# Kernel tuning notes

Measured on AMD Instinct MI355X. Metric: run time of the kernel, lower is better.

The kernel has to match this reference:

```python
import jax, jax.numpy as jnp
import numpy as np

H = 16  # n_heads


def setup_inputs() -> dict:
    key = jax.random.key(0)
    ks = jax.random.split(key, 12)
    B, S, D = 16, 512, 1024
    inp = {
        "query": jax.random.normal(ks[0], (B, S, D), jnp.float32),
        "key": jax.random.normal(ks[1], (B, S, D), jnp.float32),
        "value": jax.random.normal(ks[2], (B, S, D), jnp.float32),
        "mask": jnp.ones((B, S), dtype=bool),
        "adj": jax.random.uniform(ks[3], (B, S, S), jnp.float32),
        # nn.Linear weights are [out, in]; y = x @ W.T + b
        "Wq": jax.random.normal(ks[4], (D, D), jnp.float32) / np.sqrt(D),
        "bq": jnp.zeros((D,), jnp.float32),
        "Wk": jax.random.normal(ks[5], (D, D), jnp.float32) / np.sqrt(D),
        "bk": jnp.zeros((D,), jnp.float32),
        "Wv": jax.random.normal(ks[6], (D, D), jnp.float32) / np.sqrt(D),
        "bv": jnp.zeros((D,), jnp.float32),
        "Wo": jax.random.normal(ks[7], (D, D), jnp.float32) / np.sqrt(D),
        "bo": jnp.zeros((D,), jnp.float32),
        "beta": jnp.array([0.5], jnp.float32),  # learned residual scale (init 0 in torch)
    }
    return inp


def reference(query, key, value, mask, adj, Wq, bq, Wk, bk, Wv, bv, Wo, bo, beta):
    B, S, D = query.shape
    h = H
    dk = D // h
    N = S * dk  # channel-attention "sequence" length

    def proj(x, W, b):
        # [B,S,D] -> [B,h,S,dk]
        return (x @ W.T + b).reshape(B, S, h, dk).transpose(0, 2, 1, 3)

    Q = proj(query, Wq, bq)
    K = proj(key, Wk, bk)
    V = proj(value, Wv, bv)

    # Flatten each head: [B, h, S*dk]; torch's q,k,v are the [B,N,h] transposes.
    Qf = Q.reshape(B, h, N)
    Kf = K.reshape(B, h, N)
    Vf = V.reshape(B, h, N)

    # channel attention: scores = q^T k / sqrt(h) -> [B,h,h]
    scores = jnp.einsum("bin,bjn->bij", Qf, Kf) / jnp.sqrt(jnp.asarray(h, Qf.dtype))
    attn = jax.nn.softmax(scores, axis=-1)  # dropout is identity at eval

    # x2 = attn @ v^T -> [B,h,N] -> view [B,h,S,dk]
    x2 = jnp.einsum("bij,bjn->bin", attn, Vf).reshape(B, h, S, dk)

    x = V + beta * x2                      # scaled residual on value
    x = x.transpose(0, 2, 1, 3).reshape(B, S, D)
    out = x @ Wo.T + bo
    return out, attn
```

## Files before the change

### kernel.cpp

```cpp
#include <hip/hip_runtime.h>
#include <cstdint>
#include <cstddef>


#define DIM 1024

typedef _Float16 f16_t;
typedef _Float16 f16x4_t __attribute__((ext_vector_type(4)));
typedef _Float16 f16x8_t __attribute__((ext_vector_type(8)));
typedef float    f32x4_t __attribute__((ext_vector_type(4)));

__device__ __forceinline__ void async_ld16(const void* g, void* l) {
    __builtin_amdgcn_global_load_lds((const __attribute__((address_space(1))) void*)g,
                                     (__attribute__((address_space(3))) void*)l,
                                     16, 0, 0);
}

__global__ __launch_bounds__(256) void pack_kernel(
    const float* __restrict__ q, const float* __restrict__ k, const float* __restrict__ v,
    const float* __restrict__ Wq, const float* __restrict__ Wk,
    const float* __restrict__ Wv, const float* __restrict__ Wo,
    f16_t* __restrict__ Aq, f16_t* __restrict__ Ak, f16_t* __restrict__ Av,
    f16_t* __restrict__ Bq, f16_t* __restrict__ Bk,
    f16_t* __restrict__ Bv, f16_t* __restrict__ Bo,
    float* __restrict__ scores)
{
    const int u = blockIdx.x * 256 + threadIdx.x;
    if (u >= 7340032) {
        scores[u - 7340032] = 0.f;
        return;
    }
    const float* src; f16_t* dst; int i;
    if (u < 2097152)      { src = q;  dst = Aq; i = u; }
    else if (u < 4194304) { src = k;  dst = Ak; i = u - 2097152; }
    else if (u < 6291456) { src = v;  dst = Av; i = u - 4194304; }
    else if (u < 6553600) { src = Wq; dst = Bq; i = u - 6291456; }
    else if (u < 6815744) { src = Wk; dst = Bk; i = u - 6553600; }
    else if (u < 7077888) { src = Wv; dst = Bv; i = u - 6815744; }
    else                  { src = Wo; dst = Bo; i = u - 7077888; }
    float4 s = ((const float4*)src)[i];
    f16x4_t h;
    h[0] = (f16_t)s.x; h[1] = (f16_t)s.y; h[2] = (f16_t)s.z; h[3] = (f16_t)s.w;
    ((f16x4_t*)dst)[i] = h;
}

__device__ __forceinline__ void gemm_body(
    const f16_t* __restrict__ A, const f16_t* __restrict__ B,
    const float* __restrict__ bias, float* __restrict__ C, f16_t* __restrict__ C16,
    f16_t* As, f16_t* Bs, int tileM, int tileN)
{
    const int tid  = threadIdx.x;
    const int lane = tid & 63;
    const int w    = tid >> 6;
    const int wm = (w & 1) << 6;
    const int wn = (w >> 1) << 6;

    f32x4_t acc[4][4];
#pragma unroll
    for (int i = 0; i < 4; ++i)
#pragma unroll
        for (int j = 0; j < 4; ++j)
            acc[i][j] = (f32x4_t){0.f, 0.f, 0.f, 0.f};

    const int srow = lane >> 3;
    const int scol = ((lane & 7) ^ (lane >> 3)) << 3;
    const int arow = lane & 15;
    const int sx   = lane & 7;
    const int kqu  = lane >> 4;

    for (int kt = 0; kt < 16; ++kt) {
        const int k0 = kt << 6;
#pragma unroll
        for (int t = 0; t < 4; ++t) {
            const int row = (w << 5) + (t << 3);
            async_ld16(A + (size_t)(tileM + row + srow) * DIM + k0 + scol,
                       (void*)(As + row * 64));
            async_ld16(B + (size_t)(tileN + row + srow) * DIM + k0 + scol,
                       (void*)(Bs + row * 64));
        }
        __syncthreads();
#pragma unroll
        for (int kk = 0; kk < 2; ++kk) {
            const int cu = ((kk << 2) + kqu) ^ sx;
            f16x8_t af[4], bfv[4];
#pragma unroll
            for (int mt = 0; mt < 4; ++mt)
                af[mt] = *(const f16x8_t*)(As + (wm + (mt << 4) + arow) * 64 + (cu << 3));
#pragma unroll
            for (int nt = 0; nt < 4; ++nt)
                bfv[nt] = *(const f16x8_t*)(Bs + (wn + (nt << 4) + arow) * 64 + (cu << 3));
#pragma unroll
            for (int mt = 0; mt < 4; ++mt)
#pragma unroll
                for (int nt = 0; nt < 4; ++nt)
                    acc[mt][nt] = __builtin_amdgcn_mfma_f32_16x16x32_f16(
                        af[mt], bfv[nt], acc[mt][nt], 0, 0, 0);
        }
        __syncthreads();
    }

    const int rq = (lane >> 4) << 2;
    if (C16) {
#pragma unroll
        for (int nt = 0; nt < 4; ++nt) {
            const int col = tileN + wn + (nt << 4) + arow;
            const float bv = bias[col];
#pragma unroll
            for (int mt = 0; mt < 4; ++mt) {
                const int row = tileM + wm + (mt << 4) + rq;
#pragma unroll
                for (int r = 0; r < 4; ++r)
                    C16[(size_t)(row + r) * DIM + col] = (f16_t)(acc[mt][nt][r] + bv);
            }
        }
    } else {
#pragma unroll
        for (int nt = 0; nt < 4; ++nt) {
            const int col = tileN + wn + (nt << 4) + arow;
            const float bv = bias[col];
#pragma unroll
            for (int mt = 0; mt < 4; ++mt) {
                const int row = tileM + wm + (mt << 4) + rq;
#pragma unroll
                for (int r = 0; r < 4; ++r)
                    C[(size_t)(row + r) * DIM + col] = acc[mt][nt][r] + bv;
            }
        }
    }
}

struct Gemm3Args {
    const f16_t* A[3];
    const f16_t* B[3];
    const float* bias[3];
    float*       C[3];
    f16_t*       C16[3];
};

__global__ __launch_bounds__(256) void gemm3(Gemm3Args args)
{
    __shared__ __align__(16) f16_t As[128 * 64];
    __shared__ __align__(16) f16_t Bs[128 * 64];
    const int z = blockIdx.z;
    gemm_body(args.A[z], args.B[z], args.bias[z], args.C[z], args.C16[z],
              As, Bs, blockIdx.x * 128, blockIdx.y * 128);
}

__global__ __launch_bounds__(256) void gemm_f16(
    const f16_t* __restrict__ A, const f16_t* __restrict__ B,
    const float* __restrict__ bias, float* __restrict__ C)
{
    __shared__ __align__(16) f16_t As[128 * 64];
    __shared__ __align__(16) f16_t Bs[128 * 64];
    gemm_body(A, B, bias, C, nullptr, As, Bs, blockIdx.x * 128, blockIdx.y * 128);
}

__global__ __launch_bounds__(256) void scores_kernel(
    const f16_t* __restrict__ Pq16, const f16_t* __restrict__ Pk16,
    float* __restrict__ scores)
{
    __shared__ float red[4][256];
    const int b = blockIdx.x;
    const int lane = threadIdx.x & 63;
    const int w = threadIdx.x >> 6;
    const int m  = lane & 15;
    const int q8 = (lane >> 4) << 3;

    f32x4_t acc = (f32x4_t){0.f, 0.f, 0.f, 0.f};
    const int s0 = blockIdx.y * 16 + w * 4;
#pragma unroll
    for (int ss = 0; ss < 4; ++ss) {
        const size_t rb = (size_t)(b * 512 + s0 + ss) * DIM;
        const f16_t* qrow = Pq16 + rb;
        const f16_t* krow = Pk16 + rb;
#pragma unroll
        for (int c0 = 0; c0 < 64; c0 += 32) {
            f16x8_t af = *(const f16x8_t*)(qrow + m * 64 + c0 + q8);
            f16x8_t bf = *(const f16x8_t*)(krow + m * 64 + c0 + q8);
            acc = __builtin_amdgcn_mfma_f32_16x16x32_f16(af, bf, acc, 0, 0, 0);
        }
    }
    const int rq = (lane >> 4) << 2;
#pragma unroll
    for (int r = 0; r < 4; ++r)
        red[w][(rq + r) * 16 + m] = acc[r];
    __syncthreads();
    const int t = threadIdx.x;
    const float sum = red[0][t] + red[1][t] + red[2][t] + red[3][t];
    atomicAdd(&scores[b * 256 + t], sum);
}

__global__ __launch_bounds__(256) void softmax_kernel(
    const float* __restrict__ scores, const float* __restrict__ beta_p,
    float* __restrict__ attn_out, float* __restrict__ Mm)
{
    const int t = threadIdx.x;
    const int i = t & 15;
    const float beta = beta_p[0];
    float s[16];
    float mx = -1e30f;
#pragma unroll
    for (int j = 0; j < 16; ++j) {
        s[j] = scores[t * 16 + j] * 0.25f;
        mx = fmaxf(mx, s[j]);
    }
    float sum = 0.f;
#pragma unroll
    for (int j = 0; j < 16; ++j) { s[j] = expf(s[j] - mx); sum += s[j]; }
    const float inv = 1.f / sum;
#pragma unroll
    for (int j = 0; j < 16; ++j) {
        float a = s[j] * inv;
        attn_out[t * 16 + j] = a;
        Mm[t * 16 + j] = beta * a + ((j == i) ? 1.f : 0.f);
    }
}

__global__ __launch_bounds__(256) void mix_kernel(
    const float* __restrict__ Pv, const float* __restrict__ Mm,
    f16_t* __restrict__ xmix)
{
    __shared__ float Msh[256];
    const int rbase = blockIdx.x * 8;
    const int b = rbase >> 9;
    Msh[threadIdx.x] = Mm[b * 256 + threadIdx.x];
    __syncthreads();
    const int w = threadIdx.x >> 6;
    const int lane = threadIdx.x & 63;
#pragma unroll
    for (int rr = 0; rr < 2; ++rr) {
        const int r = rbase + w * 2 + rr;
        const float* vrow = Pv + (size_t)r * DIM;
        float v[16];
#pragma unroll
        for (int j = 0; j < 16; ++j) v[j] = vrow[j * 64 + lane];
#pragma unroll
        for (int i = 0; i < 16; ++i) {
            float x = 0.f;
#pragma unroll
            for (int j = 0; j < 16; ++j) x += Msh[i * 16 + j] * v[j];
            xmix[(size_t)r * DIM + i * 64 + lane] = (f16_t)x;
        }
    }
}

extern "C" void kernel_launch(void* const* d_in, const int* in_sizes, int n_in,
                              void* d_out, int out_size, void* d_ws, size_t ws_size,
                              hipStream_t stream)
{
    (void)in_sizes; (void)n_in; (void)out_size; (void)ws_size;
    const float* q    = (const float*)d_in[0];
    const float* k    = (const float*)d_in[1];
    const float* v    = (const float*)d_in[2];
    const float* Wq   = (const float*)d_in[5];
    const float* bq   = (const float*)d_in[6];
    const float* Wk   = (const float*)d_in[7];
    const float* bk   = (const float*)d_in[8];
    const float* Wv   = (const float*)d_in[9];
    const float* bv   = (const float*)d_in[10];
    const float* Wo   = (const float*)d_in[11];
    const float* bo   = (const float*)d_in[12];
    const float* beta = (const float*)d_in[13];

    float* out  = (float*)d_out;
    float* attn = (float*)d_out + 8388608;

    char* p = (char*)d_ws;
    auto take = [&](size_t n) -> char* {
        char* cur = p; p += (n + 255) & ~(size_t)255; return cur;
    };
    f16_t* Aq = (f16_t*)take(16777216);
    f16_t* Ak = (f16_t*)take(16777216);
    f16_t* Av = (f16_t*)take(16777216);
    f16_t* Bq = (f16_t*)take(2097152);
    f16_t* Bk = (f16_t*)take(2097152);
    f16_t* Bv = (f16_t*)take(2097152);
    f16_t* Bo = (f16_t*)take(2097152);
    f16_t* Pq16 = (f16_t*)take(16777216);
    f16_t* Pk16 = (f16_t*)take(16777216);
    float* Pv = (float*)take(33554432);
    float* scores = (float*)take(16384);
    float* Mm     = (float*)take(16384);
    f16_t* xmix = Aq;

    pack_kernel<<<28688, 256, 0, stream>>>(q, k, v, Wq, Wk, Wv, Wo,
                                           Aq, Ak, Av, Bq, Bk, Bv, Bo, scores);

    Gemm3Args ga;
    ga.A[0] = Aq; ga.A[1] = Ak; ga.A[2] = Av;
    ga.B[0] = Bq; ga.B[1] = Bk; ga.B[2] = Bv;
    ga.bias[0] = bq; ga.bias[1] = bk; ga.bias[2] = bv;
    ga.C[0] = nullptr; ga.C[1] = nullptr; ga.C[2] = Pv;
    ga.C16[0] = Pq16; ga.C16[1] = Pk16; ga.C16[2] = nullptr;
    gemm3<<<dim3(64, 8, 3), 256, 0, stream>>>(ga);

    scores_kernel<<<dim3(16, 32), 256, 0, stream>>>(Pq16, Pk16, scores);
    softmax_kernel<<<1, 256, 0, stream>>>(scores, beta, attn, Mm);
    mix_kernel<<<1024, 256, 0, stream>>>(Pv, Mm, xmix);
    gemm_f16<<<dim3(64, 8), 256, 0, stream>>>(xmix, Bo, bo, out);
}
```

Before: 293.2 us.

## Replace QKV projection GEMM with 256x256 double-buffered phased pipeline

The fused Q/K/V projection GEMM moves from 128x128 tiles with 256 threads and a single LDS buffer to 256x256 tiles with 512 threads. It double-buffers the k-slices in 128 KB of LDS and splits each k-step into four load/MFMA phases. Async global-to-LDS loads for the next tile are interleaved with MFMA work under barriers and priority hints, with explicit vmcnt waits. The aim is to hide memory latency and raise data reuse per tile, at the cost of heavier register use, larger LDS footprint, lower occupancy and fewer blocks (384) to fill the CUs.

```diff
diff --git a/kernel.cpp b/kernel.cpp
--- a/kernel.cpp
+++ b/kernel.cpp
@@ -44,69 +44,136 @@
     ((f16x4_t*)dst)[i] = h;
 }
 
-__device__ __forceinline__ void gemm_body(
-    const f16_t* __restrict__ A, const f16_t* __restrict__ B,
+__device__ __forceinline__ void gemm256_body(
+    const f16_t* __restrict__ A, const f16_t* __restrict__ Bm,
     const float* __restrict__ bias, float* __restrict__ C, f16_t* __restrict__ C16,
-    f16_t* As, f16_t* Bs, int tileM, int tileN)
+    f16_t* lds, int tileM, int tileN)
 {
     const int tid  = threadIdx.x;
     const int lane = tid & 63;
     const int w    = tid >> 6;
-    const int wm = (w & 1) << 6;
-    const int wn = (w >> 1) << 6;
-
-    f32x4_t acc[4][4];
-#pragma unroll
-    for (int i = 0; i < 4; ++i)
+    const int wm   = (w & 1) << 7;
+    const int wn   = (w >> 1) << 6;
+    const int lr   = lane & 15;
+    const int cu   = lane >> 4;
+    const int up   = (((lr & 1) << 2) | cu) ^ (lr >> 1);
+    const int abase = ((w & 1) << 12) + ((lr >> 1) << 6) + (up << 3);
+    const int bbase = ((w >> 1) << 11) + ((lr >> 1) << 6) + (up << 3);
+
+    const int su   = (tid & 7) ^ ((tid >> 3) & 7);
+    const int srow = ((tid >> 3) << 1) | (su >> 2);
+    const int sk   = (su & 3) << 3;
+    const f16_t* srcA = A  + (size_t)(tileM + srow) * DIM + sk;
+    const f16_t* srcB = Bm + (size_t)(tileN + srow) * DIM + sk;
+    f16_t* dstW = lds + (w << 9);
+
+#define STG(mat, kk, c, kt, b)  async_ld16( \
+        ((mat) ? srcB : srcA) + (size_t)(c) * 128 * DIM + (kt) * 64 + (kk) * 32, \
+        dstW + (b) * 32768 + (mat) * 16384 + (kk) * 8192 + (c) * 4096)
+
+    f32x4_t acc[8][4];
+#pragma unroll
+    for (int i = 0; i < 8; ++i)
 #pragma unroll
         for (int j = 0; j < 4; ++j)
             acc[i][j] = (f32x4_t){0.f, 0.f, 0.f, 0.f};
 
-    const int srow = lane >> 3;
-    const int scol = ((lane & 7) ^ (lane >> 3)) << 3;
-    const int arow = lane & 15;
-    const int sx   = lane & 7;
-    const int kqu  = lane >> 4;
-
+    STG(0,0,0, 0,0); STG(0,0,1, 0,0);
+    STG(1,0,0, 0,0); STG(1,0,1, 0,0);
+    STG(0,1,0, 0,0); STG(0,1,1, 0,0);
+    STG(1,1,0, 0,0); STG(1,1,1, 0,0);
+    asm volatile("s_waitcnt vmcnt(4)" ::: "memory");
+    __builtin_amdgcn_s_barrier();
+    __builtin_amdgcn_sched_barrier(0);
+
+#pragma unroll 2
     for (int kt = 0; kt < 16; ++kt) {
-        const int k0 = kt << 6;
-#pragma unroll
-        for (int t = 0; t < 4; ++t) {
-            const int row = (w << 5) + (t << 3);
-            async_ld16(A + (size_t)(tileM + row + srow) * DIM + k0 + scol,
-                       (void*)(As + row * 64));
-            async_ld16(B + (size_t)(tileN + row + srow) * DIM + k0 + scol,
-                       (void*)(Bs + row * 64));
-        }
-        __syncthreads();
-#pragma unroll
-        for (int kk = 0; kk < 2; ++kk) {
-            const int cu = ((kk << 2) + kqu) ^ sx;
-            f16x8_t af[4], bfv[4];
-#pragma unroll
-            for (int mt = 0; mt < 4; ++mt)
-                af[mt] = *(const f16x8_t*)(As + (wm + (mt << 4) + arow) * 64 + (cu << 3));
+        const int b  = kt & 1;
+        const int nb = b ^ 1;
+        const f16_t* Lb = lds + b * 32768;
+        f16x8_t af[4], bf[4];
+
+#pragma unroll
+        for (int nt = 0; nt < 4; ++nt)
+            bf[nt] = *(const f16x8_t*)(Lb + 16384 + bbase + (nt << 9));
+#pragma unroll
+        for (int mt = 0; mt < 4; ++mt)
+            af[mt] = *(const f16x8_t*)(Lb + abase + (mt << 9));
+        if (kt < 15) { STG(0,0,0, kt+1, nb); STG(0,0,1, kt+1, nb); }
+        __builtin_amdgcn_s_barrier();
+        __builtin_amdgcn_s_setprio(1);
+#pragma unroll
+        for (int mt = 0; mt < 4; ++mt)
 #pragma unroll
             for (int nt = 0; nt < 4; ++nt)
-                bfv[nt] = *(const f16x8_t*)(Bs + (wn + (nt << 4) + arow) * 64 + (cu << 3));
-#pragma unroll
-            for (int mt = 0; mt < 4; ++mt)
-#pragma unroll
-                for (int nt = 0; nt < 4; ++nt)
-                    acc[mt][nt] = __builtin_amdgcn_mfma_f32_16x16x32_f16(
-                        af[mt], bfv[nt], acc[mt][nt], 0, 0, 0);
-        }
-        __syncthreads();
-    }
+                acc[mt][nt] = __builtin_amdgcn_mfma_f32_16x16x32_f16(
+                    af[mt], bf[nt], acc[mt][nt], 0, 0, 0);
+        __builtin_amdgcn_s_setprio(0);
+        __builtin_amdgcn_s_barrier();
+
+#pragma unroll
+        for (int mt = 0; mt < 4; ++mt)
+            af[mt] = *(const f16x8_t*)(Lb + abase + ((mt + 4) << 9));
+        if (kt < 15) { STG(1,0,0, kt+1, nb); STG(1,0,1, kt+1, nb); }
+        __builtin_amdgcn_s_barrier();
+        __builtin_amdgcn_s_setprio(1);
+#pragma unroll
+        for (int mt = 0; mt < 4; ++mt)
+#pragma unroll
+            for (int nt = 0; nt < 4; ++nt)
+                acc[mt + 4][nt] = __builtin_amdgcn_mfma_f32_16x16x32_f16(
+                    af[mt], bf[nt], acc[mt + 4][nt], 0, 0, 0);
+        __builtin_amdgcn_s_setprio(0);
+        if (kt < 15) asm volatile("s_waitcnt vmcnt(4)" ::: "memory");
+        else         asm volatile("s_waitcnt vmcnt(0)" ::: "memory");
+        __builtin_amdgcn_s_barrier();
+        __builtin_amdgcn_sched_barrier(0);
+
+#pragma unroll
+        for (int nt = 0; nt < 4; ++nt)
+            bf[nt] = *(const f16x8_t*)(Lb + 24576 + bbase + (nt << 9));
+#pragma unroll
+        for (int mt = 0; mt < 4; ++mt)
+            af[mt] = *(const f16x8_t*)(Lb + 8192 + abase + (mt << 9));
+        if (kt < 15) { STG(0,1,0, kt+1, nb); STG(0,1,1, kt+1, nb); }
+        __builtin_amdgcn_s_barrier();
+        __builtin_amdgcn_s_setprio(1);
+#pragma unroll
+        for (int mt = 0; mt < 4; ++mt)
+#pragma unroll
+            for (int nt = 0; nt < 4; ++nt)
+                acc[mt][nt] = __builtin_amdgcn_mfma_f32_16x16x32_f16(
+                    af[mt], bf[nt], acc[mt][nt], 0, 0, 0);
+        __builtin_amdgcn_s_setprio(0);
+        __builtin_amdgcn_s_barrier();
+
+#pragma unroll
+        for (int mt = 0; mt < 4; ++mt)
+            af[mt] = *(const f16x8_t*)(Lb + 8192 + abase + ((mt + 4) << 9));
+        if (kt < 15) { STG(1,1,0, kt+1, nb); STG(1,1,1, kt+1, nb); }
+        __builtin_amdgcn_s_barrier();
+        __builtin_amdgcn_s_setprio(1);
+#pragma unroll
+        for (int mt = 0; mt < 4; ++mt)
+#pragma unroll
+            for (int nt = 0; nt < 4; ++nt)
+                acc[mt + 4][nt] = __builtin_amdgcn_mfma_f32_16x16x32_f16(
+                    af[mt], bf[nt], acc[mt + 4][nt], 0, 0, 0);
+        __builtin_amdgcn_s_setprio(0);
+        if (kt < 15) asm volatile("s_waitcnt vmcnt(4)" ::: "memory");
+        __builtin_amdgcn_s_barrier();
+        __builtin_amdgcn_sched_barrier(0);
+    }
+#undef STG
 
     const int rq = (lane >> 4) << 2;
     if (C16) {
 #pragma unroll
         for (int nt = 0; nt < 4; ++nt) {
-            const int col = tileN + wn + (nt << 4) + arow;
+            const int col = tileN + wn + (nt << 4) + lr;
             const float bv = bias[col];
 #pragma unroll
-            for (int mt = 0; mt < 4; ++mt) {
+            for (int mt = 0; mt < 8; ++mt) {
                 const int row = tileM + wm + (mt << 4) + rq;
 #pragma unroll
                 for (int r = 0; r < 4; ++r)
@@ -116,10 +183,10 @@
     } else {
 #pragma unroll
         for (int nt = 0; nt < 4; ++nt) {
-            const int col = tileN + wn + (nt << 4) + arow;
+            const int col = tileN + wn + (nt << 4) + lr;
             const float bv = bias[col];
 #pragma unroll
-            for (int mt = 0; mt < 4; ++mt) {
+            for (int mt = 0; mt < 8; ++mt) {
                 const int row = tileM + wm + (mt << 4) + rq;
 #pragma unroll
                 for (int r = 0; r < 4; ++r)
@@ -137,13 +204,82 @@
     f16_t*       C16[3];
 };
 
-__global__ __launch_bounds__(256) void gemm3(Gemm3Args args)
-{
-    __shared__ __align__(16) f16_t As[128 * 64];
-    __shared__ __align__(16) f16_t Bs[128 * 64];
+__global__ __launch_bounds__(512, 2) void gemm3_8ph(Gemm3Args args)
+{
+    __shared__ __align__(16) f16_t lds[65536];
     const int z = blockIdx.z;
-    gemm_body(args.A[z], args.B[z], args.bias[z], args.C[z], args.C16[z],
-              As, Bs, blockIdx.x * 128, blockIdx.y * 128);
+    gemm256_body(args.A[z], args.B[z], args.bias[z], args.C[z], args.C16[z],
+                 lds, blockIdx.x * 256, blockIdx.y * 256);
+}
+
+__device__ __forceinline__ void gemm_body(
+    const f16_t* __restrict__ A, const f16_t* __restrict__ B,
+    const float* __restrict__ bias, float* __restrict__ C, f16_t* __restrict__ C16,
+    f16_t* As, f16_t* Bs, int tileM, int tileN)
+{
+    const int tid  = threadIdx.x;
+    const int lane = tid & 63;
+    const int w    = tid >> 6;
+    const int wm = (w & 1) << 6;
+    const int wn = (w >> 1) << 6;
+
+    f32x4_t acc[4][4];
+#pragma unroll
+    for (int i = 0; i < 4; ++i)
+#pragma unroll
+        for (int j = 0; j < 4; ++j)
+            acc[i][j] = (f32x4_t){0.f, 0.f, 0.f, 0.f};
+
+    const int srow = lane >> 3;
+    const int scol = ((lane & 7) ^ (lane >> 3)) << 3;
+    const int arow = lane & 15;
+    const int sx   = lane & 7;
+    const int kqu  = lane >> 4;
+
+    for (int kt = 0; kt < 16; ++kt) {
+        const int k0 = kt << 6;
+#pragma unroll
+        for (int t = 0; t < 4; ++t) {
+            const int row = (w << 5) + (t << 3);
+            async_ld16(A + (size_t)(tileM + row + srow) * DIM + k0 + scol,
+                       (void*)(As + row * 64));
+            async_ld16(B + (size_t)(tileN + row + srow) * DIM + k0 + scol,
+                       (void*)(Bs + row * 64));
+        }
+        __syncthreads();
+#pragma unroll
+        for (int kk = 0; kk < 2; ++kk) {
+            const int cuv = ((kk << 2) + kqu) ^ sx;
+            f16x8_t af[4], bfv[4];
+#pragma unroll
+            for (int mt = 0; mt < 4; ++mt)
+                af[mt] = *(const f16x8_t*)(As + (wm + (mt << 4) + arow) * 64 + (cuv << 3));
+#pragma unroll
+            for (int nt = 0; nt < 4; ++nt)
+                bfv[nt] = *(const f16x8_t*)(Bs + (wn + (nt << 4) + arow) * 64 + (cuv << 3));
+#pragma unroll
+            for (int mt = 0; mt < 4; ++mt)
+#pragma unroll
+                for (int nt = 0; nt < 4; ++nt)
+                    acc[mt][nt] = __builtin_amdgcn_mfma_f32_16x16x32_f16(
+                        af[mt], bfv[nt], acc[mt][nt], 0, 0, 0);
+        }
+        __syncthreads();
+    }
+
+    const int rq = (lane >> 4) << 2;
+#pragma unroll
+    for (int nt = 0; nt < 4; ++nt) {
+        const int col = tileN + wn + (nt << 4) + arow;
+        const float bv = bias[col];
+#pragma unroll
+        for (int mt = 0; mt < 4; ++mt) {
+            const int row = tileM + wm + (mt << 4) + rq;
+#pragma unroll
+            for (int r = 0; r < 4; ++r)
+                C[(size_t)(row + r) * DIM + col] = acc[mt][nt][r] + bv;
+        }
+    }
 }
 
 __global__ __launch_bounds__(256) void gemm_f16(
@@ -292,7 +428,7 @@
     ga.bias[0] = bq; ga.bias[1] = bk; ga.bias[2] = bv;
     ga.C[0] = nullptr; ga.C[1] = nullptr; ga.C[2] = Pv;
     ga.C16[0] = Pq16; ga.C16[1] = Pk16; ga.C16[2] = nullptr;
-    gemm3<<<dim3(64, 8, 3), 256, 0, stream>>>(ga);
+    gemm3_8ph<<<dim3(32, 4, 3), 512, 0, stream>>>(ga);
 
     scores_kernel<<<dim3(16, 32), 256, 0, stream>>>(Pq16, Pk16, scores);
     softmax_kernel<<<1, 256, 0, stream>>>(scores, beta, attn, Mm);
```

New measurement: 295.5 us. Within noise of the previous version (+0.8%).

## Replace GEMM with 256x128 tile, 4-stage async LDS pipeline and 512 threads

Applied to the files above, without the earlier changes.

Rewrites the shared GEMM body to use 256x128 block tiles with 8 waves, a K-step of 32 and a four-buffer ring of async global-to-LDS loads issued three stages ahead. Explicit vmcnt waits replace the double __syncthreads per iteration, leaving a single barrier per step, and s_setprio raises wave priority around the MFMA block. The intent is to overlap global memory latency with MFMA work and raise arithmetic intensity per block. In exchange it uses more LDS per block, hand-coded waitcnt logic that depends on exact load counts, and half as many blocks per grid.

```diff
diff --git a/kernel.cpp b/kernel.cpp
--- a/kernel.cpp
+++ b/kernel.cpp
@@ -44,16 +44,30 @@
     ((f16x4_t*)dst)[i] = h;
 }
 
-__device__ __forceinline__ void gemm_body(
-    const f16_t* __restrict__ A, const f16_t* __restrict__ B,
+__device__ __forceinline__ void gemm256x128_body(
+    const f16_t* __restrict__ A, const f16_t* __restrict__ Bm,
     const float* __restrict__ bias, float* __restrict__ C, f16_t* __restrict__ C16,
-    f16_t* As, f16_t* Bs, int tileM, int tileN)
-{
-    const int tid  = threadIdx.x;
-    const int lane = tid & 63;
-    const int w    = tid >> 6;
-    const int wm = (w & 1) << 6;
-    const int wn = (w >> 1) << 6;
+    int tileM, int tileN)
+{
+    __shared__ __align__(16) f16_t As0[8192], As1[8192], As2[8192], As3[8192];
+    __shared__ __align__(16) f16_t Bs0[4096], Bs1[4096], Bs2[4096], Bs3[4096];
+
+    const int t    = threadIdx.x;
+    const int lane = t & 63;
+    const int w    = t >> 6;
+
+    const int srow = t >> 2;
+    const int su   = (t & 3) ^ (((t >> 2) ^ (t >> 4)) & 3);
+    const f16_t* srcA = A  + (size_t)(tileM + srow) * DIM + su * 8;
+    const f16_t* srcB = Bm + (size_t)(tileN + srow) * DIM + su * 8;
+
+    const int lr = lane & 15;
+    const int ku = lane >> 4;
+    const int uA = ku ^ ((lr ^ (lr >> 2)) & 3);
+    const int mr = w >> 1;
+    const int nr = w & 1;
+    const int aOff = mr * 2048 + lr * 32 + uA * 8;
+    const int bOff = nr * 2048 + lr * 32 + uA * 8;
 
     f32x4_t acc[4][4];
 #pragma unroll
@@ -62,52 +76,67 @@
         for (int j = 0; j < 4; ++j)
             acc[i][j] = (f32x4_t){0.f, 0.f, 0.f, 0.f};
 
-    const int srow = lane >> 3;
-    const int scol = ((lane & 7) ^ (lane >> 3)) << 3;
-    const int arow = lane & 15;
-    const int sx   = lane & 7;
-    const int kqu  = lane >> 4;
-
-    for (int kt = 0; kt < 16; ++kt) {
-        const int k0 = kt << 6;
-#pragma unroll
-        for (int t = 0; t < 4; ++t) {
-            const int row = (w << 5) + (t << 3);
-            async_ld16(A + (size_t)(tileM + row + srow) * DIM + k0 + scol,
-                       (void*)(As + row * 64));
-            async_ld16(B + (size_t)(tileN + row + srow) * DIM + k0 + scol,
-                       (void*)(Bs + row * 64));
-        }
-        __syncthreads();
-#pragma unroll
-        for (int kk = 0; kk < 2; ++kk) {
-            const int cu = ((kk << 2) + kqu) ^ sx;
-            f16x8_t af[4], bfv[4];
-#pragma unroll
-            for (int mt = 0; mt < 4; ++mt)
-                af[mt] = *(const f16x8_t*)(As + (wm + (mt << 4) + arow) * 64 + (cu << 3));
-#pragma unroll
-            for (int nt = 0; nt < 4; ++nt)
-                bfv[nt] = *(const f16x8_t*)(Bs + (wn + (nt << 4) + arow) * 64 + (cu << 3));
-#pragma unroll
-            for (int mt = 0; mt < 4; ++mt)
-#pragma unroll
-                for (int nt = 0; nt < 4; ++nt)
-                    acc[mt][nt] = __builtin_amdgcn_mfma_f32_16x16x32_f16(
-                        af[mt], bfv[nt], acc[mt][nt], 0, 0, 0);
-        }
-        __syncthreads();
-    }
-
-    const int rq = (lane >> 4) << 2;
+#define STAGE(KT, AP, BP) do {                                              \
+        const f16_t* ga_ = srcA + (KT) * 32;                                \
+        async_ld16(ga_,             (void*)((AP) + (w << 9)));              \
+        async_ld16(ga_ + 128 * DIM, (void*)((AP) + (w << 9) + 4096));       \
+        async_ld16(srcB + (KT) * 32,(void*)((BP) + (w << 9)));              \
+    } while (0)
+
+#define ITER(KT, AP, BP, PAP, PBP) do {                                     \
+        f16x8_t af_[4], bf_[4];                                             \
+        _Pragma("unroll")                                                   \
+        for (int mt = 0; mt < 4; ++mt)                                      \
+            af_[mt] = *(const f16x8_t*)((AP) + aOff + (mt << 9));           \
+        _Pragma("unroll")                                                   \
+        for (int nt = 0; nt < 4; ++nt)                                      \
+            bf_[nt] = *(const f16x8_t*)((BP) + bOff + (nt << 9));           \
+        if ((KT) < 29) STAGE((KT) + 3, PAP, PBP);                           \
+        __builtin_amdgcn_s_setprio(1);                                      \
+        _Pragma("unroll")                                                   \
+        for (int mt = 0; mt < 4; ++mt)                                      \
+        _Pragma("unroll")                                                   \
+        for (int nt = 0; nt < 4; ++nt)                                      \
+            acc[mt][nt] = __builtin_amdgcn_mfma_f32_16x16x32_f16(           \
+                af_[mt], bf_[nt], acc[mt][nt], 0, 0, 0);                    \
+        __builtin_amdgcn_s_setprio(0);                                      \
+        if ((KT) <= 28)      asm volatile("s_waitcnt vmcnt(6)" ::: "memory"); \
+        else if ((KT) == 29) asm volatile("s_waitcnt vmcnt(3)" ::: "memory"); \
+        else if ((KT) == 30) asm volatile("s_waitcnt vmcnt(0)" ::: "memory"); \
+        if ((KT) < 31) {                                                    \
+            __builtin_amdgcn_s_barrier();                                   \
+            __builtin_amdgcn_sched_barrier(0);                              \
+        }                                                                   \
+    } while (0)
+
+    STAGE(0, As0, Bs0);
+    STAGE(1, As1, Bs1);
+    STAGE(2, As2, Bs2);
+    asm volatile("s_waitcnt vmcnt(6)" ::: "memory");
+    __builtin_amdgcn_s_barrier();
+    __builtin_amdgcn_sched_barrier(0);
+
+#define QUAD(K0)                                   \
+    ITER((K0) + 0, As0, Bs0, As3, Bs3);            \
+    ITER((K0) + 1, As1, Bs1, As0, Bs0);            \
+    ITER((K0) + 2, As2, Bs2, As1, Bs1);            \
+    ITER((K0) + 3, As3, Bs3, As2, Bs2);
+
+    QUAD(0) QUAD(4) QUAD(8) QUAD(12) QUAD(16) QUAD(20) QUAD(24) QUAD(28)
+
+#undef QUAD
+#undef ITER
+#undef STAGE
+
+    const int rq = ku << 2;
     if (C16) {
 #pragma unroll
         for (int nt = 0; nt < 4; ++nt) {
-            const int col = tileN + wn + (nt << 4) + arow;
+            const int col = tileN + nr * 64 + (nt << 4) + lr;
             const float bv = bias[col];
 #pragma unroll
             for (int mt = 0; mt < 4; ++mt) {
-                const int row = tileM + wm + (mt << 4) + rq;
+                const int row = tileM + mr * 64 + (mt << 4) + rq;
 #pragma unroll
                 for (int r = 0; r < 4; ++r)
                     C16[(size_t)(row + r) * DIM + col] = (f16_t)(acc[mt][nt][r] + bv);
@@ -116,11 +145,11 @@
     } else {
 #pragma unroll
         for (int nt = 0; nt < 4; ++nt) {
-            const int col = tileN + wn + (nt << 4) + arow;
+            const int col = tileN + nr * 64 + (nt << 4) + lr;
             const float bv = bias[col];
 #pragma unroll
             for (int mt = 0; mt < 4; ++mt) {
-                const int row = tileM + wm + (mt << 4) + rq;
+                const int row = tileM + mr * 64 + (mt << 4) + rq;
 #pragma unroll
                 for (int r = 0; r < 4; ++r)
                     C[(size_t)(row + r) * DIM + col] = acc[mt][nt][r] + bv;
@@ -137,22 +166,18 @@
     f16_t*       C16[3];
 };
 
-__global__ __launch_bounds__(256) void gemm3(Gemm3Args args)
-{
-    __shared__ __align__(16) f16_t As[128 * 64];
-    __shared__ __align__(16) f16_t Bs[128 * 64];
+__global__ __launch_bounds__(512, 2) void gemm3(Gemm3Args args)
+{
     const int z = blockIdx.z;
-    gemm_body(args.A[z], args.B[z], args.bias[z], args.C[z], args.C16[z],
-              As, Bs, blockIdx.x * 128, blockIdx.y * 128);
-}
-
-__global__ __launch_bounds__(256) void gemm_f16(
+    gemm256x128_body(args.A[z], args.B[z], args.bias[z], args.C[z], args.C16[z],
+                     blockIdx.x * 256, blockIdx.y * 128);
+}
+
+__global__ __launch_bounds__(512, 2) void gemm_o(
     const f16_t* __restrict__ A, const f16_t* __restrict__ B,
     const float* __restrict__ bias, float* __restrict__ C)
 {
-    __shared__ __align__(16) f16_t As[128 * 64];
-    __shared__ __align__(16) f16_t Bs[128 * 64];
-    gemm_body(A, B, bias, C, nullptr, As, Bs, blockIdx.x * 128, blockIdx.y * 128);
+    gemm256x128_body(A, B, bias, C, nullptr, blockIdx.x * 256, blockIdx.y * 128);
 }
 
 __global__ __launch_bounds__(256) void scores_kernel(
@@ -185,9 +210,9 @@
     for (int r = 0; r < 4; ++r)
         red[w][(rq + r) * 16 + m] = acc[r];
     __syncthreads();
-    const int t = threadIdx.x;
-    const float sum = red[0][t] + red[1][t] + red[2][t] + red[3][t];
-    atomicAdd(&scores[b * 256 + t], sum);
+    const int tt = threadIdx.x;
+    const float sum = red[0][tt] + red[1][tt] + red[2][tt] + red[3][tt];
+    atomicAdd(&scores[b * 256 + tt], sum);
 }
 
 __global__ __launch_bounds__(256) void softmax_kernel(
@@ -292,10 +317,10 @@
     ga.bias[0] = bq; ga.bias[1] = bk; ga.bias[2] = bv;
     ga.C[0] = nullptr; ga.C[1] = nullptr; ga.C[2] = Pv;
     ga.C16[0] = Pq16; ga.C16[1] = Pk16; ga.C16[2] = nullptr;
-    gemm3<<<dim3(64, 8, 3), 256, 0, stream>>>(ga);
+    gemm3<<<dim3(32, 8, 3), 512, 0, stream>>>(ga);
 
     scores_kernel<<<dim3(16, 32), 256, 0, stream>>>(Pq16, Pk16, scores);
     softmax_kernel<<<1, 256, 0, stream>>>(scores, beta, attn, Mm);
     mix_kernel<<<1024, 256, 0, stream>>>(Pv, Mm, xmix);
-    gemm_f16<<<dim3(64, 8), 256, 0, stream>>>(xmix, Bo, bo, out);
-}
+    gemm_o<<<dim3(32, 8), 512, 0, stream>>>(xmix, Bo, bo, out);
+}
```

After: 289.8 us. About the same (-1.2%).

## Fuse softmax into scores kernel via last-block counter; store V projection as fp16

Applied to the files above, without the earlier changes.

Softmax is folded into the scores kernel: each block bumps an atomic counter, and the last of the 512 blocks reads the accumulated scores and writes attn and the mixing matrix. This removes a single-block kernel launch. The V projection is now written as fp16 instead of fp32, halving the write and later read traffic in the mix kernel at some precision cost. The batched 3-way projection GEMM is split into three separate launches, which adds launch overhead and gives less parallelism per launch.

```diff
diff --git a/kernel.cpp b/kernel.cpp
--- a/kernel.cpp
+++ b/kernel.cpp
@@ -27,7 +27,8 @@
 {
     const int u = blockIdx.x * 256 + threadIdx.x;
     if (u >= 7340032) {
-        scores[u - 7340032] = 0.f;
+        const int z = u - 7340032;
+        if (z < 4608) scores[z] = 0.f;
         return;
     }
     const float* src; f16_t* dst; int i;
@@ -129,24 +130,32 @@
     }
 }
 
-struct Gemm3Args {
-    const f16_t* A[3];
-    const f16_t* B[3];
-    const float* bias[3];
-    float*       C[3];
-    f16_t*       C16[3];
-};
-
-__global__ __launch_bounds__(256) void gemm3(Gemm3Args args)
+__global__ __launch_bounds__(256) void gemm_q(
+    const f16_t* __restrict__ A, const f16_t* __restrict__ B,
+    const float* __restrict__ bias, f16_t* __restrict__ C16)
 {
     __shared__ __align__(16) f16_t As[128 * 64];
     __shared__ __align__(16) f16_t Bs[128 * 64];
-    const int z = blockIdx.z;
-    gemm_body(args.A[z], args.B[z], args.bias[z], args.C[z], args.C16[z],
-              As, Bs, blockIdx.x * 128, blockIdx.y * 128);
-}
-
-__global__ __launch_bounds__(256) void gemm_f16(
+    gemm_body(A, B, bias, nullptr, C16, As, Bs, blockIdx.x * 128, blockIdx.y * 128);
+}
+__global__ __launch_bounds__(256) void gemm_k(
+    const f16_t* __restrict__ A, const f16_t* __restrict__ B,
+    const float* __restrict__ bias, f16_t* __restrict__ C16)
+{
+    __shared__ __align__(16) f16_t As[128 * 64];
+    __shared__ __align__(16) f16_t Bs[128 * 64];
+    gemm_body(A, B, bias, nullptr, C16, As, Bs, blockIdx.x * 128, blockIdx.y * 128);
+}
+__global__ __launch_bounds__(256) void gemm_v(
+    const f16_t* __restrict__ A, const f16_t* __restrict__ B,
+    const float* __restrict__ bias, f16_t* __restrict__ C16)
+{
+    __shared__ __align__(16) f16_t As[128 * 64];
+    __shared__ __align__(16) f16_t Bs[128 * 64];
+    gemm_body(A, B, bias, nullptr, C16, As, Bs, blockIdx.x * 128, blockIdx.y * 128);
+}
+
+__global__ __launch_bounds__(256) void gemm_o(
     const f16_t* __restrict__ A, const f16_t* __restrict__ B,
     const float* __restrict__ bias, float* __restrict__ C)
 {
@@ -157,9 +166,12 @@
 
 __global__ __launch_bounds__(256) void scores_kernel(
     const f16_t* __restrict__ Pq16, const f16_t* __restrict__ Pk16,
-    float* __restrict__ scores)
+    float* __restrict__ scores, int* __restrict__ counter,
+    const float* __restrict__ beta_p,
+    float* __restrict__ attn_out, float* __restrict__ Mm)
 {
     __shared__ float red[4][256];
+    __shared__ int lastflag;
     const int b = blockIdx.x;
     const int lane = threadIdx.x & 63;
     const int w = threadIdx.x >> 6;
@@ -188,26 +200,29 @@
     const int t = threadIdx.x;
     const float sum = red[0][t] + red[1][t] + red[2][t] + red[3][t];
     atomicAdd(&scores[b * 256 + t], sum);
-}
-
-__global__ __launch_bounds__(256) void softmax_kernel(
-    const float* __restrict__ scores, const float* __restrict__ beta_p,
-    float* __restrict__ attn_out, float* __restrict__ Mm)
-{
-    const int t = threadIdx.x;
+    __threadfence();
+    __syncthreads();
+    if (t == 0)
+        lastflag = (__hip_atomic_fetch_add(counter, 1, __ATOMIC_ACQ_REL,
+                                           __HIP_MEMORY_SCOPE_AGENT) == 511);
+    __syncthreads();
+    if (!lastflag) return;
+
+    __threadfence();
     const int i = t & 15;
     const float beta = beta_p[0];
     float s[16];
     float mx = -1e30f;
 #pragma unroll
     for (int j = 0; j < 16; ++j) {
-        s[j] = scores[t * 16 + j] * 0.25f;
+        s[j] = __hip_atomic_load(&scores[t * 16 + j], __ATOMIC_RELAXED,
+                                 __HIP_MEMORY_SCOPE_AGENT) * 0.25f;
         mx = fmaxf(mx, s[j]);
     }
-    float sum = 0.f;
-#pragma unroll
-    for (int j = 0; j < 16; ++j) { s[j] = expf(s[j] - mx); sum += s[j]; }
-    const float inv = 1.f / sum;
+    float ssum = 0.f;
+#pragma unroll
+    for (int j = 0; j < 16; ++j) { s[j] = expf(s[j] - mx); ssum += s[j]; }
+    const float inv = 1.f / ssum;
 #pragma unroll
     for (int j = 0; j < 16; ++j) {
         float a = s[j] * inv;
@@ -217,7 +232,7 @@
 }
 
 __global__ __launch_bounds__(256) void mix_kernel(
-    const float* __restrict__ Pv, const float* __restrict__ Mm,
+    const f16_t* __restrict__ Pv16, const float* __restrict__ Mm,
     f16_t* __restrict__ xmix)
 {
     __shared__ float Msh[256];
@@ -230,10 +245,10 @@
 #pragma unroll
     for (int rr = 0; rr < 2; ++rr) {
         const int r = rbase + w * 2 + rr;
-        const float* vrow = Pv + (size_t)r * DIM;
+        const f16_t* vrow = Pv16 + (size_t)r * DIM;
         float v[16];
 #pragma unroll
-        for (int j = 0; j < 16; ++j) v[j] = vrow[j * 64 + lane];
+        for (int j = 0; j < 16; ++j) v[j] = (float)vrow[j * 64 + lane];
 #pragma unroll
         for (int i = 0; i < 16; ++i) {
             float x = 0.f;
@@ -278,24 +293,21 @@
     f16_t* Bo = (f16_t*)take(2097152);
     f16_t* Pq16 = (f16_t*)take(16777216);
     f16_t* Pk16 = (f16_t*)take(16777216);
-    float* Pv = (float*)take(33554432);
-    float* scores = (float*)take(16384);
+    f16_t* Pv16 = (f16_t*)take(16777216);
+    float* scores = (float*)take(18688);
     float* Mm     = (float*)take(16384);
+    int*   counter = (int*)(scores + 4096);
     f16_t* xmix = Aq;
 
-    pack_kernel<<<28688, 256, 0, stream>>>(q, k, v, Wq, Wk, Wv, Wo,
+    pack_kernel<<<28690, 256, 0, stream>>>(q, k, v, Wq, Wk, Wv, Wo,
                                            Aq, Ak, Av, Bq, Bk, Bv, Bo, scores);
 
-    Gemm3Args ga;
-    ga.A[0] = Aq; ga.A[1] = Ak; ga.A[2] = Av;
-    ga.B[0] = Bq; ga.B[1] = Bk; ga.B[2] = Bv;
-    ga.bias[0] = bq; ga.bias[1] = bk; ga.bias[2] = bv;
-    ga.C[0] = nullptr; ga.C[1] = nullptr; ga.C[2] = Pv;
-    ga.C16[0] = Pq16; ga.C16[1] = Pk16; ga.C16[2] = nullptr;
-    gemm3<<<dim3(64, 8, 3), 256, 0, stream>>>(ga);
-
-    scores_kernel<<<dim3(16, 32), 256, 0, stream>>>(Pq16, Pk16, scores);
-    softmax_kernel<<<1, 256, 0, stream>>>(scores, beta, attn, Mm);
-    mix_kernel<<<1024, 256, 0, stream>>>(Pv, Mm, xmix);
-    gemm_f16<<<dim3(64, 8), 256, 0, stream>>>(xmix, Bo, bo, out);
-}
+    gemm_q<<<dim3(64, 8), 256, 0, stream>>>(Aq, Bq, bq, Pq16);
+    gemm_k<<<dim3(64, 8), 256, 0, stream>>>(Ak, Bk, bk, Pk16);
+    gemm_v<<<dim3(64, 8), 256, 0, stream>>>(Av, Bv, bv, Pv16);
+
+    scores_kernel<<<dim3(16, 32), 256, 0, stream>>>(Pq16, Pk16, scores, counter,
+                                                    beta, attn, Mm);
+    mix_kernel<<<1024, 256, 0, stream>>>(Pv16, Mm, xmix);
+    gemm_o<<<dim3(64, 8), 256, 0, stream>>>(xmix, Bo, bo, out);
+}
```

After: 338.0 us. 15.3% more time.
